# Performance work log

Measured on AMD Instinct MI355X. Metric: run time of the kernel, lower is better.

## Reference

```python
import jax, jax.numpy as jnp
import numpy as np

N = 50000
IN_CH = 128
HID = 256
HEADS = 8
HEAD_DIM = HID // HEADS
NUM_CLASSES = 2
E = 800000
NEG_SLOPE = 0.2  # PyG GATConv default leaky_relu slope


def gat_conv(x, edge_index, W, att_src, att_dst, bias):
    """PyG-style GATConv (concat=True, add_self_loops=True, eval mode).
    x: [N, HID]; edge_index: [2, E] (row 0 = source j, row 1 = target i).
    W: [HID, HEADS*HEAD_DIM]; att_src/att_dst: [HEADS, HEAD_DIM]; bias: [HEADS*HEAD_DIM].
    """
    loop = jnp.arange(N)
    src = jnp.concatenate([edge_index[0], loop])  # self-loops appended
    dst = jnp.concatenate([edge_index[1], loop])
    h = (x @ W).reshape(N, HEADS, HEAD_DIM)          # [N, H, D]
    a_src = jnp.einsum('nhd,hd->nh', h, att_src)     # [N, H]
    a_dst = jnp.einsum('nhd,hd->nh', h, att_dst)
    e = jax.nn.leaky_relu(a_src[src] + a_dst[dst], NEG_SLOPE)  # [E+N, H]
    # segment softmax over incoming edges of each target node
    m = jax.ops.segment_max(e, dst, num_segments=N)
    p = jnp.exp(e - m[dst])
    s = jax.ops.segment_sum(p, dst, num_segments=N)
    alpha = p / (s[dst] + 1e-16)                     # [E+N, H]
    msg = h[src] * alpha[:, :, None]                 # [E+N, H, D]
    out = jax.ops.segment_sum(msg, dst, num_segments=N)  # [N, H, D]
    return out.reshape(N, HEADS * HEAD_DIM) + bias


def setup_inputs() -> dict:
    key = jax.random.key(0)
    ks = jax.random.split(key, 24)
    g = lambda k, shape, fan_in: jax.random.normal(k, shape, dtype=jnp.float32) / np.sqrt(fan_in)
    inp = {}
    inp['x'] = jax.random.normal(ks[0], (N, IN_CH), dtype=jnp.float32)
    inp['tut_edge_index'] = jax.random.randint(ks[1], (2, E), 0, N)
    inp['tdt_edge_index'] = jax.random.randint(ks[2], (2, E), 0, N)
    inp['proj_W'] = g(ks[3], (IN_CH, HID), IN_CH)
    inp['proj_b'] = jnp.zeros((HID,), jnp.float32)
    # 2 GAT layers per meta-path, stacked on leading axis
    inp['tut_W'] = g(ks[4], (2, HID, HID), HID)
    inp['tut_asrc'] = g(ks[5], (2, HEADS, HEAD_DIM), HEAD_DIM)
    inp['tut_adst'] = g(ks[6], (2, HEADS, HEAD_DIM), HEAD_DIM)
    inp['tut_bias'] = jnp.zeros((2, HID), jnp.float32)
    inp['tdt_W'] = g(ks[7], (2, HID, HID), HID)
    inp['tdt_asrc'] = g(ks[8], (2, HEADS, HEAD_DIM), HEAD_DIM)
    inp['tdt_adst'] = g(ks[9], (2, HEADS, HEAD_DIM), HEAD_DIM)
    inp['tdt_bias'] = jnp.zeros((2, HID), jnp.float32)
    inp['sem_att'] = jnp.full((2,), 0.5, jnp.float32)
    inp['cls_W1'] = g(ks[10], (HID, HID // 2), HID)
    inp['cls_b1'] = jnp.zeros((HID // 2,), jnp.float32)
    inp['cls_W2'] = g(ks[11], (HID // 2, NUM_CLASSES), HID // 2)
    inp['cls_b2'] = jnp.zeros((NUM_CLASSES,), jnp.float32)
    return inp


def reference(x, tut_edge_index, tdt_edge_index, proj_W, proj_b,
              tut_W, tut_asrc, tut_adst, tut_bias,
              tdt_W, tdt_asrc, tdt_adst, tdt_bias,
              sem_att, cls_W1, cls_b1, cls_W2, cls_b2):
    h = x @ proj_W + proj_b
    # TUT branch: 2 GATConv layers (eval mode -> dropout is identity)
    h_tut = h
    for l in range(2):
        h_tut = gat_conv(h_tut, tut_edge_index, tut_W[l], tut_asrc[l], tut_adst[l], tut_bias[l])
        h_tut = jax.nn.elu(h_tut)
    # TDT branch
    h_tdt = h
    for l in range(2):
        h_tdt = gat_conv(h_tdt, tdt_edge_index, tdt_W[l], tdt_asrc[l], tdt_adst[l], tdt_bias[l])
        h_tdt = jax.nn.elu(h_tdt)
    w = jax.nn.softmax(sem_att)
    z = w[0] * h_tut + w[1] * h_tdt
    hc = jax.nn.relu(z @ cls_W1 + cls_b1)
    logits = hc @ cls_W2 + cls_b2  # [N, NUM_CLASSES]
    return logits
```

## Files before the change

### kernel.cpp

```cpp
#include <hip/hip_runtime.h>
#include <hip/hip_fp16.h>
#include <cstddef>
#include <cstdint>


#define HID        256
#define HEADS      8
#define NEG_SLOPE  0.2f

#define BSH     7
#define BNODES  128
#define MAXNB   512
#define CH      2048

typedef __attribute__((ext_vector_type(8))) short short8v;
typedef __attribute__((ext_vector_type(4))) float float4v;

static __device__ __forceinline__ unsigned short f32_to_bf16(float v) {
    union { float f; unsigned u; } c; c.f = v;
    unsigned r = c.u + 0x7FFFu + ((c.u >> 16) & 1u);
    return (unsigned short)(r >> 16);
}
static __device__ __forceinline__ float bf16_to_f32(unsigned short b) {
    union { unsigned u; float f; } c; c.u = ((unsigned)b) << 16;
    return c.f;
}
static __device__ __forceinline__ void split_bf16(float v, unsigned short& hi, unsigned short& lo) {
    hi = f32_to_bf16(v);
    lo = f32_to_bf16(v - bf16_to_f32(hi));
}
static __device__ __forceinline__ void gload_lds16(const void* g, void* l) {
    __builtin_amdgcn_global_load_lds((const __attribute__((address_space(1))) void*)g,
                                     (__attribute__((address_space(3))) void*)l, 16, 0, 0);
}

template<int MODE>
__global__ __launch_bounds__(256) void mfma_gemm_kernel(
    const unsigned short* __restrict__ Ahi, const unsigned short* __restrict__ Alo,
    const unsigned short* __restrict__ Bthi, const unsigned short* __restrict__ Btlo,
    const float* __restrict__ bias,
    unsigned short* __restrict__ Chi, unsigned short* __restrict__ Clo,
    __half* __restrict__ Cf16, float* __restrict__ Cf32,
    int M, int N, int K)
{
    __shared__ __align__(16) short lds[4 * 4096];

    const int tid  = threadIdx.x;
    const int lane = tid & 63;
    const int w    = tid >> 6;
    const int wr   = w >> 1;
    const int wc   = w & 1;
    const int m0   = blockIdx.y * 128;
    const int n0   = blockIdx.x * 128;

    const unsigned short* sbase = (w == 0) ? Ahi : (w == 1) ? Alo : (w == 2) ? Bthi : Btlo;
    const int rowbase = (w < 2) ? m0 : n0;
    const int rowlim  = ((w < 2) ? M : N) - 1;

    float4v acc[4][4];
    #pragma unroll
    for (int i = 0; i < 4; ++i)
        #pragma unroll
        for (int j = 0; j < 4; ++j)
            acc[i][j] = (float4v){0.f, 0.f, 0.f, 0.f};

    const int kcl = lane >> 4;
    const int rl  = lane & 15;

    for (int k0 = 0; k0 < K; k0 += 32) {
        #pragma unroll
        for (int rh = 0; rh < 2; ++rh) {
            int row = rowbase + rh * 64 + lane;
            row = row > rowlim ? rowlim : row;
            const unsigned short* src = sbase + (size_t)row * K + k0;
            #pragma unroll
            for (int kc = 0; kc < 4; ++kc) {
                short* dst = &lds[w * 4096 + kc * 1024 + rh * 512];
                gload_lds16(src + kc * 8, dst);
            }
        }
        __syncthreads();

        short8v ahi[4], alo[4], bhi[4], blo[4];
        #pragma unroll
        for (int i = 0; i < 4; ++i) {
            int am = wr * 64 + i * 16 + rl;
            int bn = wc * 64 + i * 16 + rl;
            ahi[i] = *(const short8v*)&lds[0 * 4096 + kcl * 1024 + am * 8];
            alo[i] = *(const short8v*)&lds[1 * 4096 + kcl * 1024 + am * 8];
            bhi[i] = *(const short8v*)&lds[2 * 4096 + kcl * 1024 + bn * 8];
            blo[i] = *(const short8v*)&lds[3 * 4096 + kcl * 1024 + bn * 8];
        }
        #pragma unroll
        for (int i = 0; i < 4; ++i)
            #pragma unroll
            for (int j = 0; j < 4; ++j) {
                acc[i][j] = __builtin_amdgcn_mfma_f32_16x16x32_bf16(ahi[i], bhi[j], acc[i][j], 0, 0, 0);
                acc[i][j] = __builtin_amdgcn_mfma_f32_16x16x32_bf16(ahi[i], blo[j], acc[i][j], 0, 0, 0);
                acc[i][j] = __builtin_amdgcn_mfma_f32_16x16x32_bf16(alo[i], bhi[j], acc[i][j], 0, 0, 0);
            }
        __syncthreads();
    }

    const int cr = (lane >> 4) * 4;
    #pragma unroll
    for (int i = 0; i < 4; ++i) {
        #pragma unroll
        for (int r = 0; r < 4; ++r) {
            int row = m0 + wr * 64 + i * 16 + cr + r;
            if (row >= M) continue;
            #pragma unroll
            for (int j = 0; j < 4; ++j) {
                int col = n0 + wc * 64 + j * 16 + rl;
                float v = acc[i][j][r];
                if (bias) v += bias[col];
                if (MODE == 0) {
                    unsigned short h, l;
                    split_bf16(v, h, l);
                    Chi[(size_t)row * N + col] = h;
                    Clo[(size_t)row * N + col] = l;
                } else if (MODE == 1) {
                    Cf16[(size_t)row * N + col] = __float2half(v);
                } else {
                    Cf32[(size_t)row * N + col] = fmaxf(v, 0.f);
                }
            }
        }
    }
}

__global__ void prep_kernel(
    const float* __restrict__ proj_W, const float* __restrict__ tut_W,
    const float* __restrict__ tdt_W, const float* __restrict__ cls_W1,
    unsigned short* __restrict__ pWthi, unsigned short* __restrict__ pWtlo,
    unsigned short* __restrict__ tWthi, unsigned short* __restrict__ tWtlo,
    unsigned short* __restrict__ dWthi, unsigned short* __restrict__ dWtlo,
    unsigned short* __restrict__ cWthi, unsigned short* __restrict__ cWtlo,
    const float* __restrict__ x,
    unsigned short* __restrict__ xhi, unsigned short* __restrict__ xlo, int count4x)
{
    const int tid = blockIdx.x * blockDim.x + threadIdx.x;
    const int stride = gridDim.x * blockDim.x;
    for (int idx = tid; idx < 327680; idx += stride) {
        unsigned short h, l;
        if (idx < 32768) {
            int k = idx >> 8, n = idx & 255;
            split_bf16(proj_W[idx], h, l);
            pWthi[n * 128 + k] = h; pWtlo[n * 128 + k] = l;
        } else if (idx < 163840) {
            int r = idx - 32768;
            int ly = r >> 16, rr = r & 65535;
            int k = rr >> 8, n = rr & 255;
            split_bf16(tut_W[r], h, l);
            tWthi[ly * 65536 + n * 256 + k] = h; tWtlo[ly * 65536 + n * 256 + k] = l;
        } else if (idx < 294912) {
            int r = idx - 163840;
            int ly = r >> 16, rr = r & 65535;
            int k = rr >> 8, n = rr & 255;
            split_bf16(tdt_W[r], h, l);
            dWthi[ly * 65536 + n * 256 + k] = h; dWtlo[ly * 65536 + n * 256 + k] = l;
        } else {
            int r = idx - 294912;
            int k = r >> 7, n = r & 127;
            split_bf16(cls_W1[r], h, l);
            cWthi[n * 256 + k] = h; cWtlo[n * 256 + k] = l;
        }
    }
    for (int i = tid; i < count4x; i += stride) {
        float4 v = reinterpret_cast<const float4*>(x)[i];
        ushort4 hh, ll;
        split_bf16(v.x, hh.x, ll.x);
        split_bf16(v.y, hh.y, ll.y);
        split_bf16(v.z, hh.z, ll.z);
        split_bf16(v.w, hh.w, ll.w);
        reinterpret_cast<ushort4*>(xhi)[i] = hh;
        reinterpret_cast<ushort4*>(xlo)[i] = ll;
    }
}

__global__ __launch_bounds__(256) void att_kernel(
    const __half* __restrict__ hW,
    const float* __restrict__ att_src, const float* __restrict__ att_dst,
    float* __restrict__ a_src, float* __restrict__ a_dst, int n_nodes)
{
    const int wave = threadIdx.x >> 6;
    const int lane = threadIdx.x & 63;
    const int n = blockIdx.x * 4 + wave;
    if (n >= n_nodes) return;

    const __half2* hp = reinterpret_cast<const __half2*>(&hW[(size_t)n * HID + lane * 4]);
    __half2 h01 = hp[0], h23 = hp[1];
    float hx = __low2float(h01), hy = __high2float(h01);
    float hz = __low2float(h23), hw = __high2float(h23);
    float4 s4 = *reinterpret_cast<const float4*>(&att_src[lane * 4]);
    float4 d4 = *reinterpret_cast<const float4*>(&att_dst[lane * 4]);
    float ps = hx * s4.x + hy * s4.y + hz * s4.z + hw * s4.w;
    float pd = hx * d4.x + hy * d4.y + hz * d4.z + hw * d4.w;
    #pragma unroll
    for (int off = 1; off < 8; off <<= 1) {
        ps += __shfl_xor(ps, off);
        pd += __shfl_xor(pd, off);
    }
    if ((lane & 7) == 0) {
        a_src[n * HEADS + (lane >> 3)] = ps;
        a_dst[n * HEADS + (lane >> 3)] = pd;
    }
}

template<int OMODE>
__global__ __launch_bounds__(256) void gat_kernel(
    const __half* __restrict__ hW,
    const float* __restrict__ a_src, const float* __restrict__ a_dst,
    const int* __restrict__ row_ptr, const int* __restrict__ adj,
    const float* __restrict__ bias,
    const unsigned short* __restrict__ prevHi, const unsigned short* __restrict__ prevLo,
    const float* __restrict__ sem,
    unsigned short* __restrict__ outhi, unsigned short* __restrict__ outlo,
    int n_nodes)
{
    const int wave = threadIdx.x >> 6;
    const int lane = threadIdx.x & 63;
    const int n = blockIdx.x * 4 + wave;
    if (n >= n_nodes) return;

    const int beg = row_ptr[n];
    const int end = row_ptr[n + 1];
    const int h2 = lane >> 3;
    const int sl = lane & 7;
    const int lane4 = lane * 4;
    const int gbase = lane & 56;

    const float adst = a_dst[n * HEADS + h2];

    float m = -INFINITY, s = 0.f;
    float4 acc = make_float4(0.f, 0.f, 0.f, 0.f);

    for (int j = beg; j < end; j += 8) {
        const int js = j + sl;
        const int valid = js < end;
        int src_l = valid ? adj[js] : 0;
        float e = -INFINITY;
        if (valid) {
            e = a_src[src_l * HEADS + h2] + adst;
            e = (e > 0.f) ? e : NEG_SLOPE * e;
        }
        float me = e;
        me = fmaxf(me, __shfl_xor(me, 1));
        me = fmaxf(me, __shfl_xor(me, 2));
        me = fmaxf(me, __shfl_xor(me, 4));
        const float m_new = fmaxf(m, me);
        const float scale = __expf(m - m_new);
        const float p = __expf(e - m_new);
        float ps = p;
        ps += __shfl_xor(ps, 1);
        ps += __shfl_xor(ps, 2);
        ps += __shfl_xor(ps, 4);
        s = s * scale + ps;
        m = m_new;
        acc.x *= scale; acc.y *= scale; acc.z *= scale; acc.w *= scale;

        #pragma unroll
        for (int jj = 0; jj < 8; ++jj) {
            if (j + jj >= end) break;
            const float alpha = __shfl(p, gbase | jj);
            const int src = __shfl(src_l, jj);
            const __half2* hp = reinterpret_cast<const __half2*>(&hW[(size_t)src * HID + lane4]);
            __half2 v01 = hp[0], v23 = hp[1];
            acc.x += alpha * __low2float(v01);
            acc.y += alpha * __high2float(v01);
            acc.z += alpha * __low2float(v23);
            acc.w += alpha * __high2float(v23);
        }
    }

    const float inv = 1.f / (s + 1e-16f);
    float4 bv = *reinterpret_cast<const float4*>(&bias[lane4]);
    float4 o;
    o.x = acc.x * inv + bv.x; o.y = acc.y * inv + bv.y;
    o.z = acc.z * inv + bv.z; o.w = acc.w * inv + bv.w;
    o.x = (o.x > 0.f) ? o.x : expm1f(o.x);
    o.y = (o.y > 0.f) ? o.y : expm1f(o.y);
    o.z = (o.z > 0.f) ? o.z : expm1f(o.z);
    o.w = (o.w > 0.f) ? o.w : expm1f(o.w);

    if (OMODE == 1) {
        const float e0 = __expf(sem[0]);
        const float e1 = __expf(sem[1]);
        const float w0 = e0 / (e0 + e1);
        const float w1 = e1 / (e0 + e1);
        ushort4 ph = *reinterpret_cast<const ushort4*>(&prevHi[(size_t)n * HID + lane4]);
        ushort4 pl = *reinterpret_cast<const ushort4*>(&prevLo[(size_t)n * HID + lane4]);
        o.x = w0 * (bf16_to_f32(ph.x) + bf16_to_f32(pl.x)) + w1 * o.x;
        o.y = w0 * (bf16_to_f32(ph.y) + bf16_to_f32(pl.y)) + w1 * o.y;
        o.z = w0 * (bf16_to_f32(ph.z) + bf16_to_f32(pl.z)) + w1 * o.z;
        o.w = w0 * (bf16_to_f32(ph.w) + bf16_to_f32(pl.w)) + w1 * o.w;
    }

    ushort4 oh, ol;
    split_bf16(o.x, oh.x, ol.x);
    split_bf16(o.y, oh.y, ol.y);
    split_bf16(o.z, oh.z, ol.z);
    split_bf16(o.w, oh.w, ol.w);
    *reinterpret_cast<ushort4*>(&outhi[(size_t)n * HID + lane4]) = oh;
    *reinterpret_cast<ushort4*>(&outlo[(size_t)n * HID + lane4]) = ol;
}

__global__ __launch_bounds__(256) void bucket_count_kernel(
    const int* __restrict__ tut_dst, const int* __restrict__ tdt_dst,
    int* __restrict__ gcount, int E, int NB)
{
    __shared__ int hist[MAXNB];
    const int g = blockIdx.y;
    const int* dstp = g ? tdt_dst : tut_dst;
    for (int i = threadIdx.x; i < MAXNB; i += 256) hist[i] = 0;
    __syncthreads();
    for (int e = blockIdx.x * 256 + threadIdx.x; e < E; e += gridDim.x * 256)
        atomicAdd(&hist[dstp[e] >> BSH], 1);
    __syncthreads();
    for (int i = threadIdx.x; i < NB; i += 256) {
        int c = hist[i];
        if (c) atomicAdd(&gcount[g * NB + i], c);
    }
}

__global__ __launch_bounds__(512) void bucket_scan_kernel(
    const int* __restrict__ gcount, int* __restrict__ ebase, int* __restrict__ adjbase,
    int* __restrict__ rp0, int* __restrict__ rp1, int N, int E, int NB)
{
    __shared__ int sa[MAXNB], sb[MAXNB];
    const int t = threadIdx.x;
    for (int g = 0; g < 2; ++g) {
        int cnt = (t < NB) ? gcount[g * NB + t] : 0;
        int nodes = 0;
        if (t < NB) { int s = t << BSH; nodes = (N - s < BNODES) ? (N - s) : BNODES; }
        sa[t] = cnt;
        sb[t] = cnt + nodes;
        __syncthreads();
        for (int off = 1; off < MAXNB; off <<= 1) {
            int va = (t >= off) ? sa[t - off] : 0;
            int vb = (t >= off) ? sb[t - off] : 0;
            __syncthreads();
            sa[t] += va; sb[t] += vb;
            __syncthreads();
        }
        if (t < NB) {
            ebase[g * (NB + 1) + t + 1] = sa[t];
            adjbase[g * (NB + 1) + t + 1] = sb[t];
        }
        if (t == 0) { ebase[g * (NB + 1)] = 0; adjbase[g * (NB + 1)] = 0; }
        __syncthreads();
    }
    if (t == 0) { rp0[N] = E + N; rp1[N] = E + N; }
}

__global__ __launch_bounds__(256) void bucket_bin_kernel(
    const int* __restrict__ tut_ei, const int* __restrict__ tdt_ei,
    const int* __restrict__ ebase, int* __restrict__ gcursor,
    int2* __restrict__ ebuf, int E, int NB)
{
    __shared__ int lhist[MAXNB];
    __shared__ int lbase[MAXNB];
    __shared__ int loffs[MAXNB];
    __shared__ int2 spair[CH];
    __shared__ int saddr[CH];
    const int g = blockIdx.y;
    const int* ei = g ? tdt_ei : tut_ei;
    const int e0 = blockIdx.x * CH;
    const int cnt = (E - e0 < CH) ? (E - e0) : CH;

    for (int i = threadIdx.x; i < MAXNB; i += 256) lhist[i] = 0;
    __syncthreads();

    int myb[8], myrank[8], mysrc[8], mydst[8];
    int nmine = 0;
    #pragma unroll
    for (int k = 0; k < 8; ++k) {
        int idx = e0 + threadIdx.x + k * 256;
        if (idx < e0 + cnt) {
            int sv = ei[idx];
            int dv = ei[E + idx];
            int b = dv >> BSH;
            int r = atomicAdd(&lhist[b], 1);
            myb[nmine] = b; myrank[nmine] = r; mysrc[nmine] = sv; mydst[nmine] = dv;
            ++nmine;
        }
    }
    __syncthreads();
    loffs[threadIdx.x] = lhist[threadIdx.x];
    loffs[threadIdx.x + 256] = lhist[threadIdx.x + 256];
    __syncthreads();
    for (int off = 1; off < MAXNB; off <<= 1) {
        int i0 = threadIdx.x, i1 = threadIdx.x + 256;
        int v0 = (i0 >= off) ? loffs[i0 - off] : 0;
        int v1 = (i1 >= off) ? loffs[i1 - off] : 0;
        __syncthreads();
        loffs[i0] += v0; loffs[i1] += v1;
        __syncthreads();
    }
    for (int i = threadIdx.x; i < NB; i += 256) {
        int c = lhist[i];
        lbase[i] = c ? atomicAdd(&gcursor[g * NB + i], c) : 0;
    }
    __syncthreads();
    const int* eb = ebase + g * (NB + 1);
    for (int k = 0; k < nmine; ++k) {
        int b = myb[k];
        int sorted = loffs[b] - lhist[b] + myrank[k];
        spair[sorted] = make_int2(mysrc[k], mydst[k]);
        saddr[sorted] = eb[b] + lbase[b] + myrank[k];
    }
    __syncthreads();
    int2* out = ebuf + (size_t)g * E;
    for (int i = threadIdx.x; i < cnt; i += 256)
        out[saddr[i]] = spair[i];
}

__global__ __launch_bounds__(256) void bucket_csr_kernel(
    const int* __restrict__ gcount, const int* __restrict__ ebase,
    const int* __restrict__ adjbase, const int2* __restrict__ ebuf,
    int* __restrict__ rp0, int* __restrict__ rp1,
    int* __restrict__ adj0, int* __restrict__ adj1, int N, int E, int NB)
{
    __shared__ int hist[BNODES], scn[BNODES], cursor[BNODES];
    const int g = blockIdx.y;
    const int b = blockIdx.x;
    int* rp  = g ? rp1 : rp0;
    int* adj = g ? adj1 : adj0;
    const int cnt = gcount[g * NB + b];
    const int aB  = adjbase[g * (NB + 1) + b];
    const int node0 = b << BSH;
    const int nb = (N - node0 < BNODES) ? (N - node0) : BNODES;
    const int2* ep = ebuf + (size_t)g * E + ebase[g * (NB + 1) + b];
    const int t = threadIdx.x;

    if (t < BNODES) hist[t] = 0;
    __syncthreads();
    for (int e = t; e < cnt; e += 256)
        atomicAdd(&hist[ep[e].y - node0], 1);
    __syncthreads();
    if (t < BNODES) scn[t] = (t < nb) ? hist[t] + 1 : 0;
    __syncthreads();
    for (int off = 1; off < BNODES; off <<= 1) {
        int v = 0;
        if (t < BNODES && t >= off) v = scn[t - off];
        __syncthreads();
        if (t < BNODES) scn[t] += v;
        __syncthreads();
    }
    if (t < nb) {
        int s = scn[t] - hist[t] - 1;
        rp[node0 + t] = aB + s;
        adj[aB + s] = node0 + t;
        cursor[t] = s + 1;
    }
    __syncthreads();
    for (int e = t; e < cnt; e += 256) {
        int2 pr = ep[e];
        int pos = atomicAdd(&cursor[pr.y - node0], 1);
        adj[aB + pos] = pr.x;
    }
}

__global__ __launch_bounds__(256) void cls2_kernel(
    const float* __restrict__ hc, const float* __restrict__ W2,
    const float* __restrict__ b2, float* __restrict__ out, int n_nodes)
{
    const int wave = threadIdx.x >> 6;
    const int lane = threadIdx.x & 63;
    const int n = blockIdx.x * 4 + wave;
    if (n >= n_nodes) return;
    float h0 = hc[(size_t)n * 128 + lane];
    float h1 = hc[(size_t)n * 128 + 64 + lane];
    float p0 = h0 * W2[lane * 2 + 0] + h1 * W2[(64 + lane) * 2 + 0];
    float p1 = h0 * W2[lane * 2 + 1] + h1 * W2[(64 + lane) * 2 + 1];
    #pragma unroll
    for (int off = 1; off < 64; off <<= 1) {
        p0 += __shfl_xor(p0, off);
        p1 += __shfl_xor(p1, off);
    }
    if (lane == 0) {
        out[(size_t)n * 2 + 0] = p0 + b2[0];
        out[(size_t)n * 2 + 1] = p1 + b2[1];
    }
}

extern "C" void kernel_launch(void* const* d_in, const int* in_sizes, int n_in,
                              void* d_out, int out_size, void* d_ws, size_t ws_size,
                              hipStream_t stream)
{
    const float* x        = (const float*)d_in[0];
    const int*   tut_ei   = (const int*)d_in[1];
    const int*   tdt_ei   = (const int*)d_in[2];
    const float* proj_W   = (const float*)d_in[3];
    const float* proj_b   = (const float*)d_in[4];
    const float* tut_W    = (const float*)d_in[5];
    const float* tut_asrc = (const float*)d_in[6];
    const float* tut_adst = (const float*)d_in[7];
    const float* tut_bias = (const float*)d_in[8];
    const float* tdt_W    = (const float*)d_in[9];
    const float* tdt_asrc = (const float*)d_in[10];
    const float* tdt_adst = (const float*)d_in[11];
    const float* tdt_bias = (const float*)d_in[12];
    const float* sem_att  = (const float*)d_in[13];
    const float* cls_W1   = (const float*)d_in[14];
    const float* cls_b1   = (const float*)d_in[15];
    const float* cls_W2   = (const float*)d_in[16];
    const float* cls_b2   = (const float*)d_in[17];

    const int IN_CH = 128;
    const int N = in_sizes[0] / IN_CH;
    const int E = in_sizes[1] / 2;
    const int NB = (N + BNODES - 1) >> BSH;
    const size_t NH = (size_t)N * HID;
    const size_t NI = (size_t)N * IN_CH;

    char* base = (char*)d_ws;
    size_t off = 0;
    auto alloc = [&](size_t bytes) -> void* {
        void* p = base + off;
        off = (off + bytes + 255) & ~(size_t)255;
        return p;
    };
    unsigned short* xhi  = (unsigned short*)alloc(NI * 2);
    unsigned short* xlo  = (unsigned short*)alloc(NI * 2);
    unsigned short* t2lo = (unsigned short*)alloc(NH * 2);
    unsigned short* h0hi = (unsigned short*)alloc(NH * 2);
    unsigned short* h0lo = (unsigned short*)alloc(NH * 2);
    unsigned short* l1hi = (unsigned short*)alloc(NH * 2);
    unsigned short* l1lo = (unsigned short*)alloc(NH * 2);
    __half*         hWf  = (__half*)alloc(NH * 2);
    float* a_src = (float*)alloc((size_t)N * HEADS * sizeof(float));
    float* a_dst = (float*)alloc((size_t)N * HEADS * sizeof(float));
    unsigned short* pWthi = (unsigned short*)alloc(256 * 128 * 2);
    unsigned short* pWtlo = (unsigned short*)alloc(256 * 128 * 2);
    unsigned short* tWthi = (unsigned short*)alloc(2 * 256 * 256 * 2);
    unsigned short* tWtlo = (unsigned short*)alloc(2 * 256 * 256 * 2);
    unsigned short* dWthi = (unsigned short*)alloc(2 * 256 * 256 * 2);
    unsigned short* dWtlo = (unsigned short*)alloc(2 * 256 * 256 * 2);
    unsigned short* cWthi = (unsigned short*)alloc(128 * 256 * 2);
    unsigned short* cWtlo = (unsigned short*)alloc(128 * 256 * 2);
    int* rp_tut  = (int*)alloc((size_t)(N + 1) * sizeof(int));
    int* adj_tut = (int*)alloc((size_t)(E + N) * sizeof(int));
    int* rp_tdt  = (int*)alloc((size_t)(N + 1) * sizeof(int));
    int* adj_tdt = (int*)alloc((size_t)(E + N) * sizeof(int));
    int* gbuf    = (int*)alloc((size_t)4 * NB * sizeof(int));
    int* gcount  = gbuf;
    int* gcursor = gbuf + 2 * NB;
    int* ebase   = (int*)alloc((size_t)2 * (NB + 1) * sizeof(int));
    int* adjbase = (int*)alloc((size_t)2 * (NB + 1) * sizeof(int));
    (void)ws_size; (void)n_in; (void)out_size;

    int2* ebuf = (int2*)hWf;
    unsigned short* t2hi = xhi;
    unsigned short* zhi  = l1hi;
    unsigned short* zlo  = l1lo;
    float*          hc   = (float*)hWf;

    const int nodeBlocks = (N + 3) / 4;

    hipMemsetAsync(gbuf, 0, (size_t)4 * NB * sizeof(int), stream);
    prep_kernel<<<1024, 256, 0, stream>>>(proj_W, tut_W, tdt_W, cls_W1,
                                          pWthi, pWtlo, tWthi, tWtlo, dWthi, dWtlo,
                                          cWthi, cWtlo, x, xhi, xlo, (int)(NI / 4));
    bucket_count_kernel<<<dim3(128, 2), 256, 0, stream>>>(tut_ei + E, tdt_ei + E, gcount, E, NB);
    bucket_scan_kernel<<<1, 512, 0, stream>>>(gcount, ebase, adjbase, rp_tut, rp_tdt, N, E, NB);
    bucket_bin_kernel<<<dim3((E + CH - 1) / CH, 2), 256, 0, stream>>>(
        tut_ei, tdt_ei, ebase, gcursor, ebuf, E, NB);
    bucket_csr_kernel<<<dim3(NB, 2), 256, 0, stream>>>(
        gcount, ebase, adjbase, ebuf, rp_tut, rp_tdt, adj_tut, adj_tdt, N, E, NB);

    const int gy = (N + 127) / 128;

    mfma_gemm_kernel<0><<<dim3(2, gy), 256, 0, stream>>>(
        xhi, xlo, pWthi, pWtlo, proj_b, h0hi, h0lo, nullptr, nullptr, N, HID, IN_CH);

    auto run_gemm_att = [&](const unsigned short* ahi, const unsigned short* alo,
                            const unsigned short* wthi, const unsigned short* wtlo,
                            const float* asrc_w, const float* adst_w) {
        mfma_gemm_kernel<1><<<dim3(2, gy), 256, 0, stream>>>(
            ahi, alo, wthi, wtlo, nullptr, nullptr, nullptr, hWf, nullptr, N, HID, HID);
        att_kernel<<<nodeBlocks, 256, 0, stream>>>(hWf, asrc_w, adst_w, a_src, a_dst, N);
    };

    const int WT = 256 * 256;
    const int AS = HEADS * (HID / HEADS);

    run_gemm_att(h0hi, h0lo, tWthi, tWtlo, tut_asrc, tut_adst);
    gat_kernel<0><<<nodeBlocks, 256, 0, stream>>>(
        hWf, a_src, a_dst, rp_tut, adj_tut, tut_bias,
        nullptr, nullptr, nullptr, l1hi, l1lo, N);
    run_gemm_att(l1hi, l1lo, tWthi + WT, tWtlo + WT, tut_asrc + AS, tut_adst + AS);
    gat_kernel<0><<<nodeBlocks, 256, 0, stream>>>(
        hWf, a_src, a_dst, rp_tut, adj_tut, tut_bias + HID,
        nullptr, nullptr, nullptr, t2hi, t2lo, N);
    run_gemm_att(h0hi, h0lo, dWthi, dWtlo, tdt_asrc, tdt_adst);
    gat_kernel<0><<<nodeBlocks, 256, 0, stream>>>(
        hWf, a_src, a_dst, rp_tdt, adj_tdt, tdt_bias,
        nullptr, nullptr, nullptr, l1hi, l1lo, N);
    run_gemm_att(l1hi, l1lo, dWthi + WT, dWtlo + WT, tdt_asrc + AS, tdt_adst + AS);
    gat_kernel<1><<<nodeBlocks, 256, 0, stream>>>(
        hWf, a_src, a_dst, rp_tdt, adj_tdt, tdt_bias + HID,
        t2hi, t2lo, sem_att, zhi, zlo, N);

    mfma_gemm_kernel<2><<<dim3(1, gy), 256, 0, stream>>>(
        zhi, zlo, cWthi, cWtlo, cls_b1, nullptr, nullptr, nullptr, hc, N, 128, HID);
    cls2_kernel<<<nodeBlocks, 256, 0, stream>>>(hc, cls_W2, cls_b2, (float*)d_out, N);
}
```

Before: 759.3 us.

## Split wave into two half-waves gathering different edges with 16-byte loads

The GAT aggregation kernel now has each half-wave of 32 lanes handle a different edge per iteration. Each lane loads 8 fp16 features (16 bytes) instead of 4, and the two halves' partial sums are combined with a cross-half shuffle at the end. The online-softmax rescale is skipped when no lane's running max increased. This is meant to raise memory-level parallelism and cut shuffle and loop overhead per edge, at the cost of more registers and an epilogue where only half the lanes write.

```diff
diff --git a/kernel.cpp b/kernel.cpp
--- a/kernel.cpp
+++ b/kernel.cpp
@@ -227,13 +227,17 @@
     const int end = row_ptr[n + 1];
     const int h2 = lane >> 3;
     const int sl = lane & 7;
-    const int lane4 = lane * 4;
-    const int gbase = lane & 56;
+    const int hw = lane >> 5;
+    const int l32 = lane & 31;
+    const int d0 = l32 * 8;
+    const int ah = (l32 >> 2) * 8;
 
     const float adst = a_dst[n * HEADS + h2];
 
     float m = -INFINITY, s = 0.f;
-    float4 acc = make_float4(0.f, 0.f, 0.f, 0.f);
+    float acc[8];
+    #pragma unroll
+    for (int k = 0; k < 8; ++k) acc[k] = 0.f;
 
     for (int j = beg; j < end; j += 8) {
         const int js = j + sl;
@@ -249,60 +253,87 @@
         me = fmaxf(me, __shfl_xor(me, 2));
         me = fmaxf(me, __shfl_xor(me, 4));
         const float m_new = fmaxf(m, me);
-        const float scale = __expf(m - m_new);
         const float p = __expf(e - m_new);
         float ps = p;
         ps += __shfl_xor(ps, 1);
         ps += __shfl_xor(ps, 2);
         ps += __shfl_xor(ps, 4);
-        s = s * scale + ps;
-        m = m_new;
-        acc.x *= scale; acc.y *= scale; acc.z *= scale; acc.w *= scale;
+        if (__any(m_new > m)) {
+            const float scale = __expf(m - m_new);
+            const float scale_g = __shfl(scale, ah);
+            s *= scale;
+            #pragma unroll
+            for (int k = 0; k < 8; ++k) acc[k] *= scale_g;
+            m = m_new;
+        }
+        s += ps;
 
         #pragma unroll
-        for (int jj = 0; jj < 8; ++jj) {
-            if (j + jj >= end) break;
-            const float alpha = __shfl(p, gbase | jj);
-            const int src = __shfl(src_l, jj);
-            const __half2* hp = reinterpret_cast<const __half2*>(&hW[(size_t)src * HID + lane4]);
-            __half2 v01 = hp[0], v23 = hp[1];
-            acc.x += alpha * __low2float(v01);
-            acc.y += alpha * __high2float(v01);
-            acc.z += alpha * __low2float(v23);
-            acc.w += alpha * __high2float(v23);
-        }
-    }
+        for (int it = 0; it < 4; ++it) {
+            const int jj = it * 2 + hw;
+            const float alpha = __shfl(p, ah | jj);
+            const int srce = __shfl(src_l, jj);
+            if (j + jj < end) {
+                float4 raw = *reinterpret_cast<const float4*>(&hW[(size_t)srce * HID + d0]);
+                __half2 v0 = *reinterpret_cast<__half2*>(&raw.x);
+                __half2 v1 = *reinterpret_cast<__half2*>(&raw.y);
+                __half2 v2 = *reinterpret_cast<__half2*>(&raw.z);
+                __half2 v3 = *reinterpret_cast<__half2*>(&raw.w);
+                acc[0] += alpha * __low2float(v0); acc[1] += alpha * __high2float(v0);
+                acc[2] += alpha * __low2float(v1); acc[3] += alpha * __high2float(v1);
+                acc[4] += alpha * __low2float(v2); acc[5] += alpha * __high2float(v2);
+                acc[6] += alpha * __low2float(v3); acc[7] += alpha * __high2float(v3);
+            }
+        }
+    }
+
+    #pragma unroll
+    for (int k = 0; k < 8; ++k) acc[k] += __shfl_xor(acc[k], 32);
 
     const float inv = 1.f / (s + 1e-16f);
-    float4 bv = *reinterpret_cast<const float4*>(&bias[lane4]);
-    float4 o;
-    o.x = acc.x * inv + bv.x; o.y = acc.y * inv + bv.y;
-    o.z = acc.z * inv + bv.z; o.w = acc.w * inv + bv.w;
-    o.x = (o.x > 0.f) ? o.x : expm1f(o.x);
-    o.y = (o.y > 0.f) ? o.y : expm1f(o.y);
-    o.z = (o.z > 0.f) ? o.z : expm1f(o.z);
-    o.w = (o.w > 0.f) ? o.w : expm1f(o.w);
-
-    if (OMODE == 1) {
-        const float e0 = __expf(sem[0]);
-        const float e1 = __expf(sem[1]);
-        const float w0 = e0 / (e0 + e1);
-        const float w1 = e1 / (e0 + e1);
-        ushort4 ph = *reinterpret_cast<const ushort4*>(&prevHi[(size_t)n * HID + lane4]);
-        ushort4 pl = *reinterpret_cast<const ushort4*>(&prevLo[(size_t)n * HID + lane4]);
-        o.x = w0 * (bf16_to_f32(ph.x) + bf16_to_f32(pl.x)) + w1 * o.x;
-        o.y = w0 * (bf16_to_f32(ph.y) + bf16_to_f32(pl.y)) + w1 * o.y;
-        o.z = w0 * (bf16_to_f32(ph.z) + bf16_to_f32(pl.z)) + w1 * o.z;
-        o.w = w0 * (bf16_to_f32(ph.w) + bf16_to_f32(pl.w)) + w1 * o.w;
-    }
-
-    ushort4 oh, ol;
-    split_bf16(o.x, oh.x, ol.x);
-    split_bf16(o.y, oh.y, ol.y);
-    split_bf16(o.z, oh.z, ol.z);
-    split_bf16(o.w, oh.w, ol.w);
-    *reinterpret_cast<ushort4*>(&outhi[(size_t)n * HID + lane4]) = oh;
-    *reinterpret_cast<ushort4*>(&outlo[(size_t)n * HID + lane4]) = ol;
+    const float inv_g = __shfl(inv, ah);
+
+    if (lane < 32) {
+        float4 b0 = *reinterpret_cast<const float4*>(&bias[d0]);
+        float4 b1 = *reinterpret_cast<const float4*>(&bias[d0 + 4]);
+        float o[8];
+        o[0] = acc[0] * inv_g + b0.x; o[1] = acc[1] * inv_g + b0.y;
+        o[2] = acc[2] * inv_g + b0.z; o[3] = acc[3] * inv_g + b0.w;
+        o[4] = acc[4] * inv_g + b1.x; o[5] = acc[5] * inv_g + b1.y;
+        o[6] = acc[6] * inv_g + b1.z; o[7] = acc[7] * inv_g + b1.w;
+        #pragma unroll
+        for (int k = 0; k < 8; ++k)
+            o[k] = (o[k] > 0.f) ? o[k] : expm1f(o[k]);
+
+        if (OMODE == 1) {
+            const float e0 = __expf(sem[0]);
+            const float e1 = __expf(sem[1]);
+            const float w0 = e0 / (e0 + e1);
+            const float w1 = e1 / (e0 + e1);
+            ushort4 ph0 = *reinterpret_cast<const ushort4*>(&prevHi[(size_t)n * HID + d0]);
+            ushort4 ph1 = *reinterpret_cast<const ushort4*>(&prevHi[(size_t)n * HID + d0 + 4]);
+            ushort4 pl0 = *reinterpret_cast<const ushort4*>(&prevLo[(size_t)n * HID + d0]);
+            ushort4 pl1 = *reinterpret_cast<const ushort4*>(&prevLo[(size_t)n * HID + d0 + 4]);
+            o[0] = w0 * (bf16_to_f32(ph0.x) + bf16_to_f32(pl0.x)) + w1 * o[0];
+            o[1] = w0 * (bf16_to_f32(ph0.y) + bf16_to_f32(pl0.y)) + w1 * o[1];
+            o[2] = w0 * (bf16_to_f32(ph0.z) + bf16_to_f32(pl0.z)) + w1 * o[2];
+            o[3] = w0 * (bf16_to_f32(ph0.w) + bf16_to_f32(pl0.w)) + w1 * o[3];
+            o[4] = w0 * (bf16_to_f32(ph1.x) + bf16_to_f32(pl1.x)) + w1 * o[4];
+            o[5] = w0 * (bf16_to_f32(ph1.y) + bf16_to_f32(pl1.y)) + w1 * o[5];
+            o[6] = w0 * (bf16_to_f32(ph1.z) + bf16_to_f32(pl1.z)) + w1 * o[6];
+            o[7] = w0 * (bf16_to_f32(ph1.w) + bf16_to_f32(pl1.w)) + w1 * o[7];
+        }
+
+        ushort4 oh0, oh1, ol0, ol1;
+        split_bf16(o[0], oh0.x, ol0.x); split_bf16(o[1], oh0.y, ol0.y);
+        split_bf16(o[2], oh0.z, ol0.z); split_bf16(o[3], oh0.w, ol0.w);
+        split_bf16(o[4], oh1.x, ol1.x); split_bf16(o[5], oh1.y, ol1.y);
+        split_bf16(o[6], oh1.z, ol1.z); split_bf16(o[7], oh1.w, ol1.w);
+        *reinterpret_cast<ushort4*>(&outhi[(size_t)n * HID + d0])     = oh0;
+        *reinterpret_cast<ushort4*>(&outhi[(size_t)n * HID + d0 + 4]) = oh1;
+        *reinterpret_cast<ushort4*>(&outlo[(size_t)n * HID + d0])     = ol0;
+        *reinterpret_cast<ushort4*>(&outlo[(size_t)n * HID + d0 + 4]) = ol1;
+    }
 }
 
 __global__ __launch_bounds__(256) void bucket_count_kernel(
```

Result: faster. 738.2 us (-2.8%).
